# Performance work log

Hardware: AMD Instinct MI355X
Metric: run time of the kernel (lower is better)

The kernel has to match this reference:

```python
import jax, jax.numpy as jnp
import numpy as np

N_NODES = 1024
N_MARBLES = 3072
N = N_NODES + N_MARBLES
N_EATERS = 64
DIM = 2
EPS = 1e-6


def setup_inputs() -> dict:
    key = jax.random.key(0)
    k1, k2, k3, k4, k5 = jax.random.split(key, 5)
    positions = jax.random.normal(k1, (N, DIM), dtype=jnp.float32) * 10.0
    velocities = jax.random.normal(k2, (N, DIM), dtype=jnp.float32)
    masses = jax.random.uniform(k3, (N,), dtype=jnp.float32) + 0.1  # strictly positive
    eater_idx = jax.random.randint(k4, (N_EATERS,), 0, N_NODES)
    eater_radius = jax.random.uniform(k5, (N_EATERS,), dtype=jnp.float32) * 0.5
    dt = jnp.ones((1,), dtype=jnp.float32) * 0.01
    return {"positions": positions, "velocities": velocities, "masses": masses,
            "eater_idx": eater_idx, "eater_radius": eater_radius, "dt": dt}


def reference(positions, velocities, masses, eater_idx, eater_radius, dt):
    # --- all-pairs net force (vectorized form of __compute_net_force_for) ---
    diff = positions[None, :, :] - positions[:, None, :]          # [N, N, D], r_j - r_i
    dist2 = jnp.sum(diff * diff, axis=-1)                          # [N, N]
    safe_d2 = jnp.where(dist2 > 0, dist2, 1.0)
    inv_d3 = jnp.where(dist2 > 0, (safe_d2 + EPS) ** -1.5, 0.0)    # excludes self (j == i)
    # gravity-style attraction: F_i = sum_j m_i m_j (r_j - r_i) / |r_j - r_i|^3
    force = jnp.einsum('i,j,ij,ijd->id', masses, masses, inv_d3, diff)  # [N, D]

    # --- update_acceleration + update_movement (semi-implicit Euler) ---
    acc = force / masses[:, None]
    vel_new = velocities + acc * dt                                # dt broadcasts from [1]
    pos_new = positions + vel_new * dt

    # --- __feed_marble_if_close_to_any_eater ---
    marble_pos = pos_new[N_NODES:]                                 # [M, D]
    eater_pos = pos_new[eater_idx]                                 # [E, D]
    d2 = jnp.sum((marble_pos[:, None, :] - eater_pos[None, :, :]) ** 2, axis=-1)  # [M, E]
    eaten = jnp.any(d2 <= (eater_radius[None, :] ** 2), axis=1)    # [M] bool

    state_new = jnp.stack([pos_new, vel_new])                      # [2, N, D]
    return state_new, eaten
```

## Files before the change

### kernel.cpp

```cpp
#include <hip/hip_runtime.h>

#define N_TOTAL   4096
#define N_NODES   1024
#define N_MARBLES 3072
#define N_EATERS  64
#define EPS       1e-6f
#define TILE      256
#define JCHUNKS   (N_TOTAL / TILE)

__global__ __launch_bounds__(TILE) void force_partial(
    const float* __restrict__ pos, const float* __restrict__ mass,
    float* __restrict__ partial)
{
    __shared__ float sx[TILE], sy[TILE], sm[TILE];
    const int i  = blockIdx.x * TILE + threadIdx.x;
    const int jc = blockIdx.y;
    const int jl = jc * TILE + threadIdx.x;

    sx[threadIdx.x] = pos[jl * 2 + 0];
    sy[threadIdx.x] = pos[jl * 2 + 1];
    sm[threadIdx.x] = mass[jl];
    __syncthreads();

    const float pxi = pos[i * 2 + 0];
    const float pyi = pos[i * 2 + 1];
    float ax = 0.f, ay = 0.f;

#pragma unroll 8
    for (int j = 0; j < TILE; ++j) {
        float dx = sx[j] - pxi;
        float dy = sy[j] - pyi;
        float d2 = dx * dx + dy * dy;
        float t  = d2 + EPS;
        float r  = rsqrtf(t);
        r = r * (1.5f - 0.5f * t * r * r);
        float w = r * r * r * sm[j];
        w = (d2 > 0.f) ? w : 0.f;
        ax = fmaf(w, dx, ax);
        ay = fmaf(w, dy, ay);
    }

    partial[(jc * N_TOTAL + i) * 2 + 0] = ax;
    partial[(jc * N_TOTAL + i) * 2 + 1] = ay;
}

__global__ __launch_bounds__(TILE) void integrate(
    const float* __restrict__ pos, const float* __restrict__ vel,
    const float* __restrict__ partial, const float* __restrict__ dtp,
    float* __restrict__ out)
{
    const int i = blockIdx.x * blockDim.x + threadIdx.x;
    const float dt = dtp[0];

    float ax = 0.f, ay = 0.f;
#pragma unroll
    for (int jc = 0; jc < JCHUNKS; ++jc) {
        ax += partial[(jc * N_TOTAL + i) * 2 + 0];
        ay += partial[(jc * N_TOTAL + i) * 2 + 1];
    }

    const float vx = vel[i * 2 + 0] + ax * dt;
    const float vy = vel[i * 2 + 1] + ay * dt;
    const float px = pos[i * 2 + 0] + vx * dt;
    const float py = pos[i * 2 + 1] + vy * dt;

    out[i * 2 + 0] = px;
    out[i * 2 + 1] = py;
    out[2 * N_TOTAL + i * 2 + 0] = vx;
    out[2 * N_TOTAL + i * 2 + 1] = vy;
}

__global__ __launch_bounds__(TILE) void eaten_kernel(
    const float* __restrict__ out_state, const int* __restrict__ eater_idx,
    const float* __restrict__ eater_radius, float* __restrict__ out_eaten)
{
    __shared__ float ex[N_EATERS], ey[N_EATERS], er2[N_EATERS];
    if (threadIdx.x < N_EATERS) {
        const int idx = eater_idx[threadIdx.x];
        ex[threadIdx.x] = out_state[idx * 2 + 0];
        ey[threadIdx.x] = out_state[idx * 2 + 1];
        const float r = eater_radius[threadIdx.x];
        er2[threadIdx.x] = r * r;
    }
    __syncthreads();

    const int m = blockIdx.x * blockDim.x + threadIdx.x;
    const float mx = out_state[(N_NODES + m) * 2 + 0];
    const float my = out_state[(N_NODES + m) * 2 + 1];

    bool any = false;
#pragma unroll
    for (int e = 0; e < N_EATERS; ++e) {
        const float dx = mx - ex[e];
        const float dy = my - ey[e];
        any = any || (dx * dx + dy * dy <= er2[e]);
    }
    out_eaten[m] = any ? 1.0f : 0.0f;
}

extern "C" void kernel_launch(void* const* d_in, const int* in_sizes, int n_in,
                              void* d_out, int out_size, void* d_ws, size_t ws_size,
                              hipStream_t stream) {
    const float* pos  = (const float*)d_in[0];
    const float* vel  = (const float*)d_in[1];
    const float* mass = (const float*)d_in[2];
    const int*   eidx = (const int*)d_in[3];
    const float* erad = (const float*)d_in[4];
    const float* dt   = (const float*)d_in[5];

    float* out     = (float*)d_out;
    float* partial = (float*)d_ws;

    dim3 g1(N_TOTAL / TILE, JCHUNKS);
    force_partial<<<g1, TILE, 0, stream>>>(pos, mass, partial);
    integrate<<<N_TOTAL / TILE, TILE, 0, stream>>>(pos, vel, partial, dt, out);
    eaten_kernel<<<N_MARBLES / TILE, TILE, 0, stream>>>(out, eidx, erad,
                                                        out + 4 * N_TOTAL);
}
```

Before: 86.92 us.

## Split force j-range into smaller chunks, drop shared tile and Newton refinement

Shrinks the per-block j-range from 256 to 64. This quadruples the number of force blocks so the 256-CU device gets more waves in flight. Each thread now reads j positions and masses straight from global memory as wave-uniform loads instead of staging them in shared memory behind a barrier. The Newton-Raphson refinement of rsqrt and the explicit d2>0 self mask are removed; the self term vanishes anyway because dx=dy=0. The integrate kernel now sums 64 partials with float2 loads, so the partial buffer and the reduction traffic grow, and accuracy rests on the hardware rsqrt alone.

```diff
diff --git a/kernel.cpp b/kernel.cpp
--- a/kernel.cpp
+++ b/kernel.cpp
@@ -5,46 +5,37 @@
 #define N_MARBLES 3072
 #define N_EATERS  64
 #define EPS       1e-6f
-#define TILE      256
-#define JCHUNKS   (N_TOTAL / TILE)
+#define BLOCK     256
+#define JCHUNK    64
+#define JCHUNKS   (N_TOTAL / JCHUNK)
 
-__global__ __launch_bounds__(TILE) void force_partial(
+__global__ __launch_bounds__(BLOCK) void force_partial(
     const float* __restrict__ pos, const float* __restrict__ mass,
     float* __restrict__ partial)
 {
-    __shared__ float sx[TILE], sy[TILE], sm[TILE];
-    const int i  = blockIdx.x * TILE + threadIdx.x;
-    const int jc = blockIdx.y;
-    const int jl = jc * TILE + threadIdx.x;
-
-    sx[threadIdx.x] = pos[jl * 2 + 0];
-    sy[threadIdx.x] = pos[jl * 2 + 1];
-    sm[threadIdx.x] = mass[jl];
-    __syncthreads();
+    const int i  = blockIdx.x * BLOCK + threadIdx.x;
+    const int j0 = blockIdx.y * JCHUNK;
 
     const float pxi = pos[i * 2 + 0];
     const float pyi = pos[i * 2 + 1];
     float ax = 0.f, ay = 0.f;
 
-#pragma unroll 8
-    for (int j = 0; j < TILE; ++j) {
-        float dx = sx[j] - pxi;
-        float dy = sy[j] - pyi;
-        float d2 = dx * dx + dy * dy;
-        float t  = d2 + EPS;
-        float r  = rsqrtf(t);
-        r = r * (1.5f - 0.5f * t * r * r);
-        float w = r * r * r * sm[j];
-        w = (d2 > 0.f) ? w : 0.f;
+#pragma unroll 16
+    for (int j = j0; j < j0 + JCHUNK; ++j) {
+        const float dx = pos[j * 2 + 0] - pxi;
+        const float dy = pos[j * 2 + 1] - pyi;
+        const float t  = fmaf(dx, dx, fmaf(dy, dy, EPS));
+        const float r  = rsqrtf(t);
+        const float w  = r * r * r * mass[j];
         ax = fmaf(w, dx, ax);
         ay = fmaf(w, dy, ay);
     }
 
-    partial[(jc * N_TOTAL + i) * 2 + 0] = ax;
-    partial[(jc * N_TOTAL + i) * 2 + 1] = ay;
+    partial[(blockIdx.y * N_TOTAL + i) * 2 + 0] = ax;
+    partial[(blockIdx.y * N_TOTAL + i) * 2 + 1] = ay;
 }
 
-__global__ __launch_bounds__(TILE) void integrate(
+__global__ __launch_bounds__(BLOCK) void integrate(
     const float* __restrict__ pos, const float* __restrict__ vel,
     const float* __restrict__ partial, const float* __restrict__ dtp,
     float* __restrict__ out)
@@ -52,11 +43,13 @@
     const int i = blockIdx.x * blockDim.x + threadIdx.x;
     const float dt = dtp[0];
 
+    const float2* __restrict__ p2 = (const float2*)partial;
     float ax = 0.f, ay = 0.f;
-#pragma unroll
+#pragma unroll 16
     for (int jc = 0; jc < JCHUNKS; ++jc) {
-        ax += partial[(jc * N_TOTAL + i) * 2 + 0];
-        ay += partial[(jc * N_TOTAL + i) * 2 + 1];
+        const float2 p = p2[jc * N_TOTAL + i];
+        ax += p.x;
+        ay += p.y;
     }
 
     const float vx = vel[i * 2 + 0] + ax * dt;
@@ -70,7 +63,7 @@
     out[2 * N_TOTAL + i * 2 + 1] = vy;
 }
 
-__global__ __launch_bounds__(TILE) void eaten_kernel(
+__global__ __launch_bounds__(BLOCK) void eaten_kernel(
     const float* __restrict__ out_state, const int* __restrict__ eater_idx,
     const float* __restrict__ eater_radius, float* __restrict__ out_eaten)
 {
@@ -111,9 +104,9 @@
     float* out     = (float*)d_out;
     float* partial = (float*)d_ws;
 
-    dim3 g1(N_TOTAL / TILE, JCHUNKS);
-    force_partial<<<g1, TILE, 0, stream>>>(pos, mass, partial);
-    integrate<<<N_TOTAL / TILE, TILE, 0, stream>>>(pos, vel, partial, dt, out);
-    eaten_kernel<<<N_MARBLES / TILE, TILE, 0, stream>>>(out, eidx, erad,
-                                                        out + 4 * N_TOTAL);
+    dim3 g1(N_TOTAL / BLOCK, JCHUNKS);
+    force_partial<<<g1, BLOCK, 0, stream>>>(pos, mass, partial);
+    integrate<<<N_TOTAL / BLOCK, BLOCK, 0, stream>>>(pos, vel, partial, dt, out);
+    eaten_kernel<<<N_MARBLES / BLOCK, BLOCK, 0, stream>>>(out, eidx, erad,
+                                                          out + 4 * N_TOTAL);
 }
```

Result: faster. 79.63 us (-8.4%).
